# Optimization experiments

Measured on AMD Instinct MI355X. Metric: run time of the kernel, lower is better.

## Reference

```python
import jax, jax.numpy as jnp
import numpy as np

SMOOTH = 1.0
EPS = 1e-8
K_SKEL = 50  # soft_skel default; module's self.k is unused in forward


def _max_pool3d(x, w):
    # x: (b, c, D, H, W); w: 3-tuple window; stride 1, 'same'-style padding (k-1)//2
    window = (1, 1) + tuple(w)
    pad = [(0, 0), (0, 0)] + [((k - 1) // 2, (k - 1) // 2) for k in w]
    return jax.lax.reduce_window(x, -jnp.inf, jax.lax.max, window, (1,) * 5, pad)


def soft_erode(I):
    p1 = -_max_pool3d(-I, (3, 1, 1))
    p2 = -_max_pool3d(-I, (1, 3, 1))
    p3 = -_max_pool3d(-I, (1, 1, 3))
    return jnp.minimum(jnp.minimum(p1, p3), p2)


def soft_dilate(I):
    return _max_pool3d(I, (3, 3, 3))


def soft_open(I):
    return soft_dilate(soft_erode(I))


def soft_skel(img, k=K_SKEL):
    skel = jax.nn.relu(img - soft_open(img))

    @jax.checkpoint
    def body(carry, _):
        img, skel = carry
        img = soft_erode(img)
        delta = jax.nn.relu(img - soft_open(img))
        skel = skel + jax.nn.relu(delta - skel * delta)
        return (img, skel), None

    (_, skel), _ = jax.lax.scan(body, (img, skel), None, length=k)
    return skel


def setup_inputs() -> dict:
    key = jax.random.key(0)
    kx, ky = jax.random.split(key)
    shape = (2, 2, 80, 80, 80)
    x = jax.random.uniform(kx, shape, dtype=jnp.float32)
    y = jax.random.uniform(ky, shape, dtype=jnp.float32)
    return {"x": x, "y": y}


def reference(x, y):
    # batch_dice=False -> reduce over spatial axes only
    axes = (2, 3, 4)
    clp = soft_skel(x)
    cll = soft_skel(y)
    # shapes equal -> y_onehot is the soft target itself
    tp = jnp.sum(x * cll, axis=axes)             # (b, c)
    fn = jnp.sum((1.0 - x) * cll, axis=axes)
    tpc = jnp.sum(clp * y, axis=axes)
    fpc = jnp.sum(clp * (1.0 - y), axis=axes)
    clp2voll = (tpc + SMOOTH) / (tpc + fpc + SMOOTH)
    cll2volp = (tp + SMOOTH) / (tp + fn + SMOOTH)
    dc = 2.0 * clp2voll * cll2volp / (cll2volp + clp2voll + EPS)
    return 1.0 - dc.mean()  # do_bg=True -> no channel slicing
```

## Files before the change

### kernel.cpp

```cpp
#include <hip/hip_runtime.h>

#define DDIM 80
#define PLANE 6400
#define VOL 512000
#define HALFV 4
#define NVOL 8
#define NTOT (NVOL*VOL)

#define TY 10
#define CZ 5
#define NYT 8
#define NZC 16
#define NCH 20
#define RP 84
#define ER (TY + 2)
#define BLK 256
#define GRID (NVOL*NYT*NZC)

__device__ __forceinline__ float4 f4min(float4 a, float4 b) {
    return make_float4(fminf(a.x,b.x), fminf(a.y,b.y), fminf(a.z,b.z), fminf(a.w,b.w));
}
__device__ __forceinline__ float4 f4max(float4 a, float4 b) {
    return make_float4(fmaxf(a.x,b.x), fmaxf(a.y,b.y), fmaxf(a.z,b.z), fmaxf(a.w,b.w));
}
__device__ __forceinline__ int slotE(int v){ return (v + 9) % 3; }
__device__ __forceinline__ int slotH(int v){ return (v + 8) & 3; }
__device__ __forceinline__ float updf(float s, float d){ return s + fmaxf(d - s*d, 0.0f); }

__device__ __forceinline__ void lbar() {
    asm volatile("s_waitcnt lgkmcnt(0)\n\ts_barrier" ::: "memory");
}

struct EIn { float4 c, zA, zB, yA, yB; float lf, rt; };

template<bool FIRST, bool LASTK>
__global__ __launch_bounds__(BLK, 4) void iter_k(const float* __restrict__ xin,
                                                 const float* __restrict__ yin,
                                                 const float* __restrict__ a,
                                                 float* __restrict__ eout,
                                                 float* __restrict__ skel)
{
    __shared__ float E[3][ER][RP];
    __shared__ float H[4][ER][RP];

    const int b = blockIdx.x;
    const int v   = b >> 7;
    const int rem = b & 127;
    const int yt  = rem >> 4;
    const int zci = rem & 15;
    const int y0 = yt*TY;
    const int z0 = zci*CZ;

    const float* __restrict__ src =
        FIRST ? ((v < HALFV) ? (xin + v*VOL) : (yin + (v-HALFV)*VOL)) : (a + v*VOL);
    float* __restrict__ ev = LASTK ? nullptr : (eout + v*VOL);
    float* __restrict__ skv = skel + v*VOL;

    const int tid = threadIdx.x;
    const int r = tid / NCH;
    const int c = tid - r*NCH;
    const int x4 = 4*c;

    auto loadE = [&](int zs, EIn& e) {
        if (tid < ER*NCH) {
            const int gy  = y0 - 1 + r;
            const int gyc = min(max(gy, 0), DDIM-1);
            const int zcl = min(max(zs, 0), DDIM-1);
            const int zm = max(zcl-1, 0), zp = min(zcl+1, DDIM-1);
            const int ym = max(gyc-1, 0), yp = min(gyc+1, DDIM-1);
            const float* rc = src + zcl*PLANE + gyc*DDIM;
            e.c  = *(const float4*)(rc + x4);
            e.lf = rc[max(x4-1, 0)];
            e.rt = rc[min(x4+4, DDIM-1)];
            e.zA = *(const float4*)(src + zm*PLANE + gyc*DDIM + x4);
            e.zB = *(const float4*)(src + zp*PLANE + gyc*DDIM + x4);
            e.yA = *(const float4*)(src + zcl*PLANE + ym*DDIM + x4);
            e.yB = *(const float4*)(src + zcl*PLANE + yp*DDIM + x4);
        }
    };

    auto erodeCompute = [&](const EIn& e) -> float4 {
        float4 m;
        m.x = fminf(fminf(e.lf,  e.c.x), e.c.y);
        m.y = fminf(fminf(e.c.x, e.c.y), e.c.z);
        m.z = fminf(fminf(e.c.y, e.c.z), e.c.w);
        m.w = fminf(fminf(e.c.z, e.c.w), e.rt);
        return f4min(m, f4min(f4min(e.zA, e.zB), f4min(e.yA, e.yB)));
    };

    auto storeE = [&](int zs, const float4& m) {
        if (tid < ER*NCH) {
            *(float4*)&E[slotE(zs)][r][x4] = m;
            if constexpr (!LASTK) {
                if (r >= 1 && r <= TY && zs >= z0 && zs < z0 + CZ)
                    *(float4*)(ev + zs*PLANE + (y0 + r - 1)*DDIM + x4) = m;
            }
        }
    };

    auto hmaxStore = [&](int zs, const float4& m) {
        if (tid < ER*NCH) {
            const float* er = &E[slotE(zs)][r][0];
            const float lf = (c > 0)  ? er[x4-1] : m.x;
            const float rt = (c < 19) ? er[x4+4] : m.w;
            float4 h;
            h.x = fmaxf(fmaxf(lf,  m.x), m.y);
            h.y = fmaxf(fmaxf(m.x, m.y), m.z);
            h.z = fmaxf(fmaxf(m.y, m.z), m.w);
            h.w = fmaxf(fmaxf(m.z, m.w), rt);
            *(float4*)&H[slotH(zs)][r][x4] = h;
        }
    };

    auto loadD = [&](int z, float4& img, float4& sk) {
        if (tid < TY*NCH) {
            const int off = z*PLANE + (y0 + r)*DDIM + x4;
            img = *(const float4*)(src + off);
            if constexpr (!FIRST) sk = *(const float4*)(skv + off);
        }
    };

    auto dilateUpd = [&](int z, const float4& img, const float4& skin) {
        if (tid < TY*NCH) {
            const int ss[3] = {slotH(z-1), slotH(z), slotH(z+1)};
            float4 dm = make_float4(-1e30f, -1e30f, -1e30f, -1e30f);
#pragma unroll
            for (int s = 0; s < 3; ++s)
#pragma unroll
                for (int l = 0; l < 3; ++l)
                    dm = f4max(dm, *(const float4*)&H[ss[s]][r + l][x4]);

            float4 dl;
            dl.x = fmaxf(img.x - dm.x, 0.0f);
            dl.y = fmaxf(img.y - dm.y, 0.0f);
            dl.z = fmaxf(img.z - dm.z, 0.0f);
            dl.w = fmaxf(img.w - dm.w, 0.0f);
            float4 s;
            if constexpr (FIRST) {
                s = dl;
            } else {
                s = skin;
                s.x = updf(s.x, dl.x); s.y = updf(s.y, dl.y);
                s.z = updf(s.z, dl.z); s.w = updf(s.w, dl.w);
            }
            *(float4*)(skv + z*PLANE + (y0 + r)*DDIM + x4) = s;
        }
    };

    EIn eP, eQ, eR;
    float4 m0, m1, m2, mPrev, mNew;
    float4 dImg, dSk, dImgN, dSkN;

    loadE(z0-1, eP);
    loadE(z0,   eQ);
    loadE(z0+1, eR);
    m0 = erodeCompute(eP);  storeE(z0-1, m0);
    m1 = erodeCompute(eQ);  storeE(z0,   m1);
    lbar();

    loadE(z0+2, eP);
    loadE(z0+3, eQ);
    hmaxStore(z0-1, m0);
    hmaxStore(z0,   m1);
    m2 = erodeCompute(eR);  storeE(z0+1, m2);
    loadD(z0, dImg, dSk);
    lbar();
    mPrev = m2;

#pragma unroll
    for (int S = 0; S < CZ; ++S) {
        const int z = z0 + S;
        if (S <= CZ-2) {
            mNew = erodeCompute((S & 1) ? eQ : eP);
            storeE(z+2, mNew);
        }
        if (S <= CZ-4) loadE(z+4, (S & 1) ? eQ : eP);
        hmaxStore(z+1, mPrev);
        if (S <= CZ-2) loadD(z+1, dImgN, dSkN);
        lbar();
        dilateUpd(z, dImg, dSk);
        if (S <= CZ-2) { mPrev = mNew; dImg = dImgN; dSk = dSkN; }
    }
}

__global__ __launch_bounds__(256) void reduce_k(const float* __restrict__ x,
                                                const float* __restrict__ y,
                                                const float* __restrict__ skel,
                                                float* __restrict__ partials) {
    const int blk = blockIdx.x;
    const int v = blk >> 8;
    const int sub = blk & 255;
    const int base4 = (v * VOL + sub * 2000) >> 2;
    const float4* x4 = (const float4*)x;
    const float4* y4 = (const float4*)y;
    const float4* clp4 = (const float4*)(skel);
    const float4* cll4 = (const float4*)(skel + HALFV * VOL);
    float s1 = 0, s2 = 0, s3 = 0, s4 = 0;
    for (int j = threadIdx.x; j < 500; j += 256) {
        const int i4 = base4 + j;
        const float4 xv = x4[i4];
        const float4 yv = y4[i4];
        const float4 cp = clp4[i4];
        const float4 cl = cll4[i4];
        s1 += xv.x*cl.x + xv.y*cl.y + xv.z*cl.z + xv.w*cl.w;
        s2 += cl.x + cl.y + cl.z + cl.w;
        s3 += cp.x*yv.x + cp.y*yv.y + cp.z*yv.z + cp.w*yv.w;
        s4 += cp.x + cp.y + cp.z + cp.w;
    }
    for (int off = 32; off > 0; off >>= 1) {
        s1 += __shfl_down(s1, off);
        s2 += __shfl_down(s2, off);
        s3 += __shfl_down(s3, off);
        s4 += __shfl_down(s4, off);
    }
    __shared__ float smm[4][4];
    const int wave = threadIdx.x >> 6;
    if ((threadIdx.x & 63) == 0) {
        smm[wave][0] = s1; smm[wave][1] = s2; smm[wave][2] = s3; smm[wave][3] = s4;
    }
    __syncthreads();
    if (threadIdx.x == 0) {
        float a0 = 0, a1 = 0, a2 = 0, a3 = 0;
        for (int w = 0; w < 4; ++w) { a0 += smm[w][0]; a1 += smm[w][1]; a2 += smm[w][2]; a3 += smm[w][3]; }
        partials[blk*4 + 0] = a0;
        partials[blk*4 + 1] = a1;
        partials[blk*4 + 2] = a2;
        partials[blk*4 + 3] = a3;
    }
}

__global__ void final_k(const float* __restrict__ p, float* __restrict__ out) {
    __shared__ float sums[16];
    const int t = threadIdx.x;
    if (t < 16) {
        const int v = t >> 2, k = t & 3;
        float acc = 0.0f;
        for (int b = 0; b < 256; ++b) acc += p[((v << 8) + b)*4 + k];
        sums[t] = acc;
    }
    __syncthreads();
    if (t == 0) {
        float acc = 0.0f;
        for (int v = 0; v < 4; ++v) {
            const float tp      = sums[v*4 + 0];
            const float sum_cll = sums[v*4 + 1];
            const float tpc     = sums[v*4 + 2];
            const float sum_clp = sums[v*4 + 3];
            const float fn  = sum_cll - tp;
            const float fpc = sum_clp - tpc;
            const float clp2voll = (tpc + 1.0f) / (tpc + fpc + 1.0f);
            const float cll2volp = (tp + 1.0f) / (tp + fn + 1.0f);
            acc += 2.0f * clp2voll * cll2volp / (cll2volp + clp2voll + 1e-8f);
        }
        out[0] = 1.0f - acc * 0.25f;
    }
}

extern "C" void kernel_launch(void* const* d_in, const int* in_sizes, int n_in,
                              void* d_out, int out_size, void* d_ws, size_t ws_size,
                              hipStream_t stream) {
    const float* x = (const float*)d_in[0];
    const float* y = (const float*)d_in[1];
    float* out = (float*)d_out;

    float* bufA = (float*)d_ws;
    float* bufB = bufA + NTOT;
    float* skel = bufB + NTOT;
    float* partials = skel + NTOT;

    iter_k<true, false><<<GRID, BLK, 0, stream>>>(x, y, nullptr, bufA, skel);
    for (int t = 1; t <= 49; ++t) {
        iter_k<false, false><<<GRID, BLK, 0, stream>>>(nullptr, nullptr, bufA, bufB, skel);
        float* tmp = bufA; bufA = bufB; bufB = tmp;
    }
    iter_k<false, true><<<GRID, BLK, 0, stream>>>(nullptr, nullptr, bufA, nullptr, skel);

    reduce_k<<<1024, 256, 0, stream>>>(x, y, skel, partials);
    final_k<<<1, 64, 0, stream>>>(partials, out);
}
```

Measured before the change: 845.3 us.

## Fuse two skeleton iterations per kernel launch with temporal blocking

```diff
diff --git a/kernel.cpp b/kernel.cpp
--- a/kernel.cpp
+++ b/kernel.cpp
@@ -6,16 +6,24 @@
 #define HALFV 4
 #define NVOL 8
 #define NTOT (NVOL*VOL)
-
-#define TY 10
-#define CZ 5
-#define NYT 8
-#define NZC 16
 #define NCH 20
 #define RP 84
-#define ER (TY + 2)
 #define BLK 256
-#define GRID (NVOL*NYT*NZC)
+
+#define PTY 8
+#define PCZ 10
+#define PE1R 12
+#define PHR 10
+#define PNYT 10
+#define PNZC 8
+#define PGRID (NVOL*PNYT*PNZC)
+
+#define STY 10
+#define SCZ 5
+#define SNYT 8
+#define SNZC 16
+#define SER (STY + 2)
+#define SGRID (NVOL*SNYT*SNZC)
 
 __device__ __forceinline__ float4 f4min(float4 a, float4 b) {
     return make_float4(fminf(a.x,b.x), fminf(a.y,b.y), fminf(a.z,b.z), fminf(a.w,b.w));
@@ -23,8 +31,8 @@
 __device__ __forceinline__ float4 f4max(float4 a, float4 b) {
     return make_float4(fmaxf(a.x,b.x), fmaxf(a.y,b.y), fmaxf(a.z,b.z), fmaxf(a.w,b.w));
 }
-__device__ __forceinline__ int slotE(int v){ return (v + 9) % 3; }
-__device__ __forceinline__ int slotH(int v){ return (v + 8) & 3; }
+__device__ __forceinline__ int s4(int v){ return (v + 8) & 3; }
+__device__ __forceinline__ int s2(int v){ return (v + 8) & 1; }
 __device__ __forceinline__ float updf(float s, float d){ return s + fmaxf(d - s*d, 0.0f); }
 
 __device__ __forceinline__ void lbar() {
@@ -32,6 +40,209 @@
 }
 
 struct EIn { float4 c, zA, zB, yA, yB; float lf, rt; };
+
+template<bool FIRST>
+__global__ __launch_bounds__(BLK, 3) void pair_k(const float* __restrict__ xin,
+                                                 const float* __restrict__ yin,
+                                                 const float* __restrict__ a,
+                                                 float* __restrict__ eout,
+                                                 float* __restrict__ skel)
+{
+    __shared__ float E1[4][PE1R][RP];
+    __shared__ float H1[4][PHR][RP];
+    __shared__ float E2[2][PHR][RP];
+    __shared__ float H2[4][PHR][RP];
+
+    const int b = blockIdx.x;
+    const int v   = b / (PNYT*PNZC);
+    const int rem = b - v*(PNYT*PNZC);
+    const int yt  = rem / PNZC;
+    const int zci = rem - yt*PNZC;
+    const int y0 = yt*PTY;
+    const int z0 = zci*PCZ;
+
+    const float* __restrict__ src =
+        FIRST ? ((v < HALFV) ? (xin + v*VOL) : (yin + (v-HALFV)*VOL)) : (a + v*VOL);
+    float* __restrict__ ev  = eout + v*VOL;
+    float* __restrict__ skv = skel + v*VOL;
+
+    const int tid = threadIdx.x;
+    const int r = tid / NCH;
+    const int c = tid - r*NCH;
+    const int x4 = 4*c;
+
+    auto loadE1 = [&](int zs, EIn& e) {
+        if (r < PE1R) {
+            const int gy  = y0 - 2 + r;
+            const int gyc = min(max(gy, 0), DDIM-1);
+            const int zcl = min(max(zs, 0), DDIM-1);
+            const int zm = max(zcl-1, 0), zp = min(zcl+1, DDIM-1);
+            const int ym = max(gyc-1, 0), yp = min(gyc+1, DDIM-1);
+            const float* rc = src + zcl*PLANE + gyc*DDIM;
+            e.c  = *(const float4*)(rc + x4);
+            e.lf = rc[max(x4-1, 0)];
+            e.rt = rc[min(x4+4, DDIM-1)];
+            e.zA = *(const float4*)(src + zm*PLANE + gyc*DDIM + x4);
+            e.zB = *(const float4*)(src + zp*PLANE + gyc*DDIM + x4);
+            e.yA = *(const float4*)(src + zcl*PLANE + ym*DDIM + x4);
+            e.yB = *(const float4*)(src + zcl*PLANE + yp*DDIM + x4);
+        }
+    };
+
+    auto erodeC = [&](const EIn& e) -> float4 {
+        float4 m;
+        m.x = fminf(fminf(e.lf,  e.c.x), e.c.y);
+        m.y = fminf(fminf(e.c.x, e.c.y), e.c.z);
+        m.z = fminf(fminf(e.c.y, e.c.z), e.c.w);
+        m.w = fminf(fminf(e.c.z, e.c.w), e.rt);
+        return f4min(m, f4min(f4min(e.zA, e.zB), f4min(e.yA, e.yB)));
+    };
+
+    auto storeE1 = [&](int zs, float4 m) {
+        if (r < PE1R) *(float4*)&E1[s4(zs)][r][x4] = m;
+    };
+
+    auto hmax1 = [&](int zs) {
+        if (r < PHR) {
+            const float* row = &E1[s4(zs)][r+1][0];
+            const float4 f = *(const float4*)(row + x4);
+            const float lf = (c>0)  ? row[x4-1] : f.x;
+            const float rt = (c<19) ? row[x4+4] : f.w;
+            float4 h;
+            h.x = fmaxf(fmaxf(lf,  f.x), f.y);
+            h.y = fmaxf(fmaxf(f.x, f.y), f.z);
+            h.z = fmaxf(fmaxf(f.y, f.z), f.w);
+            h.w = fmaxf(fmaxf(f.z, f.w), rt);
+            *(float4*)&H1[s4(zs)][r][x4] = h;
+        }
+    };
+
+    auto erode2 = [&](int zs, bool gw) {
+        if (r < PHR) {
+            const float* rc = &E1[s4(zs)][r+1][0];
+            const float4 cc = *(const float4*)(rc + x4);
+            const float lf = (c>0)  ? rc[x4-1] : cc.x;
+            const float rt = (c<19) ? rc[x4+4] : cc.w;
+            float4 m;
+            m.x = fminf(fminf(lf,   cc.x), cc.y);
+            m.y = fminf(fminf(cc.x, cc.y), cc.z);
+            m.z = fminf(fminf(cc.y, cc.z), cc.w);
+            m.w = fminf(fminf(cc.z, cc.w), rt);
+            m = f4min(m, *(const float4*)&E1[s4(zs)][r][x4]);
+            m = f4min(m, *(const float4*)&E1[s4(zs)][r+2][x4]);
+            m = f4min(m, *(const float4*)&E1[s4(zs-1)][r+1][x4]);
+            m = f4min(m, *(const float4*)&E1[s4(zs+1)][r+1][x4]);
+            *(float4*)&E2[s2(zs)][r][x4] = m;
+            if (gw && r >= 1 && r <= PTY)
+                *(float4*)(ev + zs*PLANE + (y0-1+r)*DDIM + x4) = m;
+        }
+    };
+
+    auto hmax2 = [&](int zs) {
+        if (r < PHR) {
+            const float* row = &E2[s2(zs)][r][0];
+            const float4 f = *(const float4*)(row + x4);
+            const float lf = (c>0)  ? row[x4-1] : f.x;
+            const float rt = (c<19) ? row[x4+4] : f.w;
+            float4 h;
+            h.x = fmaxf(fmaxf(lf,  f.x), f.y);
+            h.y = fmaxf(fmaxf(f.x, f.y), f.z);
+            h.z = fmaxf(fmaxf(f.y, f.z), f.w);
+            h.w = fmaxf(fmaxf(f.z, f.w), rt);
+            *(float4*)&H2[s4(zs)][r][x4] = h;
+        }
+    };
+
+    auto loadD1 = [&](int z, float4& img, float4& sk) {
+        if (r < PTY) {
+            const int off = z*PLANE + (y0 + r)*DDIM + x4;
+            img = *(const float4*)(src + off);
+            if constexpr (!FIRST) sk = *(const float4*)(skv + off);
+        }
+    };
+
+    EIn eS0, eS1;
+    float4 img2N = make_float4(0,0,0,0), img2P = make_float4(0,0,0,0);
+    float4 skA = make_float4(0,0,0,0), skB = skA, skC = skA;
+    float4 dImg = skA, dSk = skA;
+
+    loadE1(z0-2, eS0);
+    loadE1(z0-1, eS1);
+    storeE1(z0-2, erodeC(eS0));
+    storeE1(z0-1, erodeC(eS1));
+    loadE1(z0,   eS0);
+    loadE1(z0+1, eS1);
+    lbar();
+    storeE1(z0,   erodeC(eS0));
+    storeE1(z0+1, erodeC(eS1));
+    hmax1(z0-1);
+    loadE1(z0+2, eS1);
+    lbar();
+    hmax1(z0);
+    erode2(z0-1, false);
+    loadE1(z0+3, eS0);
+    lbar();
+
+#pragma unroll
+    for (int S = -1; S <= PCZ; ++S) {
+        const int z = z0 + S;
+        if (S <= PCZ-2) {
+            const float4 m = erodeC((S & 1) ? eS1 : eS0);
+            storeE1(z+3, m);
+        }
+        if (S <= PCZ-4) loadE1(z+5, (S & 1) ? eS1 : eS0);
+        if (S <= PCZ-2) hmax1(z+2);
+        if (S <= PCZ-1) erode2(z+1, S <= PCZ-2);
+        hmax2(z);
+        if (S >= 0 && S <= PCZ-1) {
+            if (r < PTY) img2N = *(const float4*)&E1[s4(z)][r+2][x4];
+        }
+        if (S <= PCZ-2) loadD1(z+1, dImg, dSk);
+        lbar();
+        if (S <= PCZ-2) {
+            if (r < PTY) {
+                float4 dm = make_float4(-1e30f, -1e30f, -1e30f, -1e30f);
+#pragma unroll
+                for (int s = 0; s < 3; ++s)
+#pragma unroll
+                    for (int l = 0; l < 3; ++l)
+                        dm = f4max(dm, *(const float4*)&H1[s4(z+s)][r + l][x4]);
+                float4 dl;
+                dl.x = fmaxf(dImg.x - dm.x, 0.0f);
+                dl.y = fmaxf(dImg.y - dm.y, 0.0f);
+                dl.z = fmaxf(dImg.z - dm.z, 0.0f);
+                dl.w = fmaxf(dImg.w - dm.w, 0.0f);
+                if constexpr (FIRST) {
+                    skC = dl;
+                } else {
+                    skC.x = updf(dSk.x, dl.x); skC.y = updf(dSk.y, dl.y);
+                    skC.z = updf(dSk.z, dl.z); skC.w = updf(dSk.w, dl.w);
+                }
+            }
+        }
+        if (S >= 1) {
+            if (r < PTY) {
+                float4 dm = make_float4(-1e30f, -1e30f, -1e30f, -1e30f);
+#pragma unroll
+                for (int s = 0; s < 3; ++s)
+#pragma unroll
+                    for (int l = 0; l < 3; ++l)
+                        dm = f4max(dm, *(const float4*)&H2[s4(z-2+s)][r + l][x4]);
+                float4 dl;
+                dl.x = fmaxf(img2P.x - dm.x, 0.0f);
+                dl.y = fmaxf(img2P.y - dm.y, 0.0f);
+                dl.z = fmaxf(img2P.z - dm.z, 0.0f);
+                dl.w = fmaxf(img2P.w - dm.w, 0.0f);
+                float4 sf;
+                sf.x = updf(skA.x, dl.x); sf.y = updf(skA.y, dl.y);
+                sf.z = updf(skA.z, dl.z); sf.w = updf(skA.w, dl.w);
+                *(float4*)(skv + (z-1)*PLANE + (y0 + r)*DDIM + x4) = sf;
+            }
+        }
+        skA = skB; skB = skC;
+        img2P = img2N;
+    }
+}
 
 template<bool FIRST, bool LASTK>
 __global__ __launch_bounds__(BLK, 4) void iter_k(const float* __restrict__ xin,
@@ -40,16 +251,16 @@
                                                  float* __restrict__ eout,
                                                  float* __restrict__ skel)
 {
-    __shared__ float E[3][ER][RP];
-    __shared__ float H[4][ER][RP];
+    __shared__ float E[3][SER][RP];
+    __shared__ float H[4][SER][RP];
 
     const int b = blockIdx.x;
     const int v   = b >> 7;
     const int rem = b & 127;
     const int yt  = rem >> 4;
     const int zci = rem & 15;
-    const int y0 = yt*TY;
-    const int z0 = zci*CZ;
+    const int y0 = yt*STY;
+    const int z0 = zci*SCZ;
 
     const float* __restrict__ src =
         FIRST ? ((v < HALFV) ? (xin + v*VOL) : (yin + (v-HALFV)*VOL)) : (a + v*VOL);
@@ -61,8 +272,10 @@
     const int c = tid - r*NCH;
     const int x4 = 4*c;
 
+    auto slotE = [](int vv){ return (vv + 9) % 3; };
+
     auto loadE = [&](int zs, EIn& e) {
-        if (tid < ER*NCH) {
+        if (tid < SER*NCH) {
             const int gy  = y0 - 1 + r;
             const int gyc = min(max(gy, 0), DDIM-1);
             const int zcl = min(max(zs, 0), DDIM-1);
@@ -78,8 +291,7 @@
             e.yB = *(const float4*)(src + zcl*PLANE + yp*DDIM + x4);
         }
     };
-
-    auto erodeCompute = [&](const EIn& e) -> float4 {
+    auto erodeC = [&](const EIn& e) -> float4 {
         float4 m;
         m.x = fminf(fminf(e.lf,  e.c.x), e.c.y);
         m.y = fminf(fminf(e.c.x, e.c.y), e.c.z);
@@ -87,19 +299,17 @@
         m.w = fminf(fminf(e.c.z, e.c.w), e.rt);
         return f4min(m, f4min(f4min(e.zA, e.zB), f4min(e.yA, e.yB)));
     };
-
     auto storeE = [&](int zs, const float4& m) {
-        if (tid < ER*NCH) {
+        if (tid < SER*NCH) {
             *(float4*)&E[slotE(zs)][r][x4] = m;
             if constexpr (!LASTK) {
-                if (r >= 1 && r <= TY && zs >= z0 && zs < z0 + CZ)
+                if (r >= 1 && r <= STY && zs >= z0 && zs < z0 + SCZ)
                     *(float4*)(ev + zs*PLANE + (y0 + r - 1)*DDIM + x4) = m;
             }
         }
     };
-
     auto hmaxStore = [&](int zs, const float4& m) {
-        if (tid < ER*NCH) {
+        if (tid < SER*NCH) {
             const float* er = &E[slotE(zs)][r][0];
             const float lf = (c > 0)  ? er[x4-1] : m.x;
             const float rt = (c < 19) ? er[x4+4] : m.w;
@@ -108,37 +318,32 @@
             h.y = fmaxf(fmaxf(m.x, m.y), m.z);
             h.z = fmaxf(fmaxf(m.y, m.z), m.w);
             h.w = fmaxf(fmaxf(m.z, m.w), rt);
-            *(float4*)&H[slotH(zs)][r][x4] = h;
-        }
-    };
-
+            *(float4*)&H[s4(zs)][r][x4] = h;
+        }
+    };
     auto loadD = [&](int z, float4& img, float4& sk) {
-        if (tid < TY*NCH) {
+        if (tid < STY*NCH) {
             const int off = z*PLANE + (y0 + r)*DDIM + x4;
             img = *(const float4*)(src + off);
             if constexpr (!FIRST) sk = *(const float4*)(skv + off);
         }
     };
-
     auto dilateUpd = [&](int z, const float4& img, const float4& skin) {
-        if (tid < TY*NCH) {
-            const int ss[3] = {slotH(z-1), slotH(z), slotH(z+1)};
+        if (tid < STY*NCH) {
             float4 dm = make_float4(-1e30f, -1e30f, -1e30f, -1e30f);
 #pragma unroll
             for (int s = 0; s < 3; ++s)
 #pragma unroll
                 for (int l = 0; l < 3; ++l)
-                    dm = f4max(dm, *(const float4*)&H[ss[s]][r + l][x4]);
-
+                    dm = f4max(dm, *(const float4*)&H[s4(z-1+s)][r + l][x4]);
             float4 dl;
             dl.x = fmaxf(img.x - dm.x, 0.0f);
             dl.y = fmaxf(img.y - dm.y, 0.0f);
             dl.z = fmaxf(img.z - dm.z, 0.0f);
             dl.w = fmaxf(img.w - dm.w, 0.0f);
             float4 s;
-            if constexpr (FIRST) {
-                s = dl;
-            } else {
+            if constexpr (FIRST) { s = dl; }
+            else {
                 s = skin;
                 s.x = updf(s.x, dl.x); s.y = updf(s.y, dl.y);
                 s.z = updf(s.z, dl.z); s.w = updf(s.w, dl.w);
@@ -154,32 +359,31 @@
     loadE(z0-1, eP);
     loadE(z0,   eQ);
     loadE(z0+1, eR);
-    m0 = erodeCompute(eP);  storeE(z0-1, m0);
-    m1 = erodeCompute(eQ);  storeE(z0,   m1);
+    m0 = erodeC(eP);  storeE(z0-1, m0);
+    m1 = erodeC(eQ);  storeE(z0,   m1);
     lbar();
-
     loadE(z0+2, eP);
     loadE(z0+3, eQ);
     hmaxStore(z0-1, m0);
     hmaxStore(z0,   m1);
-    m2 = erodeCompute(eR);  storeE(z0+1, m2);
+    m2 = erodeC(eR);  storeE(z0+1, m2);
     loadD(z0, dImg, dSk);
     lbar();
     mPrev = m2;
 
 #pragma unroll
-    for (int S = 0; S < CZ; ++S) {
+    for (int S = 0; S < SCZ; ++S) {
         const int z = z0 + S;
-        if (S <= CZ-2) {
-            mNew = erodeCompute((S & 1) ? eQ : eP);
+        if (S <= SCZ-2) {
+            mNew = erodeC((S & 1) ? eQ : eP);
             storeE(z+2, mNew);
         }
-        if (S <= CZ-4) loadE(z+4, (S & 1) ? eQ : eP);
+        if (S <= SCZ-4) loadE(z+4, (S & 1) ? eQ : eP);
         hmaxStore(z+1, mPrev);
-        if (S <= CZ-2) loadD(z+1, dImgN, dSkN);
+        if (S <= SCZ-2) loadD(z+1, dImgN, dSkN);
         lbar();
         dilateUpd(z, dImg, dSk);
-        if (S <= CZ-2) { mPrev = mNew; dImg = dImgN; dSk = dSkN; }
+        if (S <= SCZ-2) { mPrev = mNew; dImg = dImgN; dSk = dSkN; }
     }
 }
 
@@ -195,7 +399,7 @@
     const float4* y4 = (const float4*)y;
     const float4* clp4 = (const float4*)(skel);
     const float4* cll4 = (const float4*)(skel + HALFV * VOL);
-    float s1 = 0, s2 = 0, s3 = 0, s4 = 0;
+    float s1 = 0, s2 = 0, s3 = 0, s4_ = 0;
     for (int j = threadIdx.x; j < 500; j += 256) {
         const int i4 = base4 + j;
         const float4 xv = x4[i4];
@@ -205,18 +409,18 @@
         s1 += xv.x*cl.x + xv.y*cl.y + xv.z*cl.z + xv.w*cl.w;
         s2 += cl.x + cl.y + cl.z + cl.w;
         s3 += cp.x*yv.x + cp.y*yv.y + cp.z*yv.z + cp.w*yv.w;
-        s4 += cp.x + cp.y + cp.z + cp.w;
+        s4_ += cp.x + cp.y + cp.z + cp.w;
     }
     for (int off = 32; off > 0; off >>= 1) {
         s1 += __shfl_down(s1, off);
         s2 += __shfl_down(s2, off);
         s3 += __shfl_down(s3, off);
-        s4 += __shfl_down(s4, off);
+        s4_ += __shfl_down(s4_, off);
     }
     __shared__ float smm[4][4];
     const int wave = threadIdx.x >> 6;
     if ((threadIdx.x & 63) == 0) {
-        smm[wave][0] = s1; smm[wave][1] = s2; smm[wave][2] = s3; smm[wave][3] = s4;
+        smm[wave][0] = s1; smm[wave][1] = s2; smm[wave][2] = s3; smm[wave][3] = s4_;
     }
     __syncthreads();
     if (threadIdx.x == 0) {
@@ -268,12 +472,13 @@
     float* skel = bufB + NTOT;
     float* partials = skel + NTOT;
 
-    iter_k<true, false><<<GRID, BLK, 0, stream>>>(x, y, nullptr, bufA, skel);
-    for (int t = 1; t <= 49; ++t) {
-        iter_k<false, false><<<GRID, BLK, 0, stream>>>(nullptr, nullptr, bufA, bufB, skel);
-        float* tmp = bufA; bufA = bufB; bufB = tmp;
-    }
-    iter_k<false, true><<<GRID, BLK, 0, stream>>>(nullptr, nullptr, bufA, nullptr, skel);
+    pair_k<true><<<PGRID, BLK, 0, stream>>>(x, y, nullptr, bufA, skel);
+    for (int j = 1; j <= 24; ++j) {
+        float* srcb = (j & 1) ? bufA : bufB;
+        float* dstb = (j & 1) ? bufB : bufA;
+        pair_k<false><<<PGRID, BLK, 0, stream>>>(nullptr, nullptr, srcb, dstb, skel);
+    }
+    iter_k<false, true><<<SGRID, BLK, 0, stream>>>(nullptr, nullptr, bufA, nullptr, skel);
 
     reduce_k<<<1024, 256, 0, stream>>>(x, y, skel, partials);
     final_k<<<1, 64, 0, stream>>>(partials, out);
```

New measurement: 724.5 us. 14.3% less time.
